# Kernel tuning notes

Measured on AMD Instinct MI355X. Metric: run time of the kernel, lower is better.

The kernel has to match this reference:

```python
import jax, jax.numpy as jnp
import numpy as np

B, S, D = 2, 2048, 1024
H = 16
HD = D // H  # 64
SCALE = HD ** -0.5


def setup_inputs() -> dict:
    key = jax.random.key(0)
    ks = jax.random.split(key, 9)
    init = lambda k, shape: jax.random.normal(k, shape, dtype=jnp.float32) * (1.0 / np.sqrt(shape[-1]))
    return {
        "x": jax.random.normal(ks[0], (B, S, D), dtype=jnp.float32),
        "wq": init(ks[1], (D, D)), "bq": jnp.zeros((D,), jnp.float32),
        "wk": init(ks[2], (D, D)), "bk": jnp.zeros((D,), jnp.float32),
        "wv": init(ks[3], (D, D)), "bv": jnp.zeros((D,), jnp.float32),
        "wo": init(ks[4], (D, D)), "bo": jnp.zeros((D,), jnp.float32),
    }


def reference(x, wq, bq, wk, bk, wv, bv, wo, bo):
    b, s, d = x.shape
    # projections -> [b, h, s, hd]
    q = (x @ wq + bq).reshape(b, s, H, HD).transpose(0, 2, 1, 3)
    k = (x @ wk + bk).reshape(b, s, H, HD).transpose(0, 2, 1, 3)
    v = (x @ wv + bv).reshape(b, s, H, HD).transpose(0, 2, 1, 3)
    # full causal attention (chunked loop in original computes exactly this)
    scores = jnp.einsum("bhqd,bhkd->bhqk", q, k) * SCALE
    causal = jnp.tril(jnp.ones((s, s), dtype=bool))
    scores = jnp.where(causal, scores, -jnp.inf)
    weights = jax.nn.softmax(scores, axis=-1)
    out = jnp.einsum("bhqk,bhkd->bhqd", weights, v)
    out = out.transpose(0, 2, 1, 3).reshape(b, s, d)
    return out @ wo + bo
```

## Files before the change

kernel.cpp:

```cpp
#include <hip/hip_runtime.h>
#include <hip/hip_bf16.h>
#include <cstdint>

#define B_  2
#define S_  2048
#define D_  1024
#define H_  16
#define HD_ 64
#define M_  (B_ * S_)
static constexpr float SC_LOG2E = 0.125f * 1.44269504088896f;

typedef __bf16 bf16x8 __attribute__((ext_vector_type(8)));
typedef float  f32x4  __attribute__((ext_vector_type(4)));

__device__ __forceinline__ unsigned short f2b(float f) {
  union { float f; unsigned u; } x; x.f = f;
  unsigned r = x.u + 0x7FFF + ((x.u >> 16) & 1);
  return (unsigned short)(r >> 16);
}

__device__ __forceinline__ void gl_lds16(const unsigned short* g, unsigned short* l) {
  __builtin_amdgcn_global_load_lds((const __attribute__((address_space(1))) void*)g,
                                   (__attribute__((address_space(3))) void*)l, 16, 0, 0);
}

__global__ void cvt_all_kernel(const float* __restrict__ x,
                               const float* __restrict__ w0, const float* __restrict__ w1,
                               const float* __restrict__ w2, const float* __restrict__ w3,
                               unsigned short* __restrict__ xb,
                               unsigned short* __restrict__ o0, unsigned short* __restrict__ o1,
                               unsigned short* __restrict__ o2, unsigned short* __restrict__ o3) {
  int tx = threadIdx.x, ty = threadIdx.y;
  if (blockIdx.z == 4) {
    int tid = ty * 32 + tx;
    int base = ((int)blockIdx.y * 32 + (int)blockIdx.x) * 1024 + tid;
    const float4* xf = (const float4*)x;
    ushort4* ob = (ushort4*)xb;
#pragma unroll
    for (int j = 0; j < 4; j++) {
      float4 v = xf[base + j * 256];
      ushort4 r;
      r.x = f2b(v.x); r.y = f2b(v.y); r.z = f2b(v.z); r.w = f2b(v.w);
      ob[base + j * 256] = r;
    }
    return;
  }
  const float* w = blockIdx.z == 0 ? w0 : blockIdx.z == 1 ? w1 : blockIdx.z == 2 ? w2 : w3;
  unsigned short* o = blockIdx.z == 0 ? o0 : blockIdx.z == 1 ? o1 : blockIdx.z == 2 ? o2 : o3;
  __shared__ float t[32][33];
  int x0 = blockIdx.x * 32, y0 = blockIdx.y * 32;
#pragma unroll
  for (int j = 0; j < 4; j++)
    t[ty + j * 8][tx] = w[(size_t)(y0 + ty + j * 8) * D_ + x0 + tx];
  __syncthreads();
#pragma unroll
  for (int j = 0; j < 4; j++)
    o[(size_t)(x0 + ty + j * 8) * D_ + y0 + tx] = f2b(t[tx][ty + j * 8]);
}

__global__ __launch_bounds__(256) void qkv_gemm_kernel(
    const unsigned short* __restrict__ xb,
    const unsigned short* __restrict__ wqt, const unsigned short* __restrict__ wkt,
    const unsigned short* __restrict__ wvt,
    const float* __restrict__ bq, const float* __restrict__ bk, const float* __restrict__ bv,
    unsigned short* __restrict__ qo, unsigned short* __restrict__ ko, unsigned short* __restrict__ vo) {
  const unsigned short* wt = blockIdx.z == 0 ? wqt : blockIdx.z == 1 ? wkt : wvt;
  const float* bias        = blockIdx.z == 0 ? bq  : blockIdx.z == 1 ? bk  : bv;
  unsigned short* out      = blockIdx.z == 0 ? qo  : blockIdx.z == 1 ? ko  : vo;
  const float scl = blockIdx.z == 0 ? SC_LOG2E : 1.0f;

  __shared__ __align__(16) unsigned short As[128 * 32];
  __shared__ __align__(16) unsigned short Bs[128 * 32];
  const int tid = threadIdx.x;
  const int lane = tid & 63, wid = tid >> 6;
  const int wm = wid & 1, wn = wid >> 1;
  const int m0 = blockIdx.x * 128, n0 = blockIdx.y * 128;
  const int l15 = lane & 15, q4 = lane >> 4;

  f32x4 zero = {0.f, 0.f, 0.f, 0.f};
  f32x4 acc[4][4];
#pragma unroll
  for (int mt = 0; mt < 4; mt++)
#pragma unroll
    for (int nt = 0; nt < 4; nt++) acc[mt][nt] = zero;

  for (int kk = 0; kk < D_; kk += 32) {
#pragma unroll
    for (int i = 0; i < 2; i++) {
      int ci = tid + i * 256;
      int row = ci >> 2, kc = ci & 3;
      gl_lds16(xb + (size_t)(m0 + row) * D_ + kk + kc * 8, As + ci * 8);
      gl_lds16(wt + (size_t)(n0 + row) * D_ + kk + kc * 8, Bs + ci * 8);
    }
    __syncthreads();
    bf16x8 af[4], bfv[4];
#pragma unroll
    for (int mt = 0; mt < 4; mt++) af[mt] = *(const bf16x8*)(As + (wm * 64 + mt * 16 + l15) * 32 + q4 * 8);
#pragma unroll
    for (int nt = 0; nt < 4; nt++) bfv[nt] = *(const bf16x8*)(Bs + (wn * 64 + nt * 16 + l15) * 32 + q4 * 8);
#pragma unroll
    for (int mt = 0; mt < 4; mt++)
#pragma unroll
      for (int nt = 0; nt < 4; nt++)
        acc[mt][nt] = __builtin_amdgcn_mfma_f32_16x16x32_bf16(af[mt], bfv[nt], acc[mt][nt], 0, 0, 0);
    __syncthreads();
  }

  if (blockIdx.z < 2) {
#pragma unroll
    for (int nt = 0; nt < 4; nt++) {
      int n = n0 + wn * 64 + nt * 16 + l15;
      float bn = bias[n];
      int h = n >> 6, hd = n & 63;
#pragma unroll
      for (int mt = 0; mt < 4; mt++) {
#pragma unroll
        for (int r = 0; r < 4; r++) {
          int m = m0 + wm * 64 + mt * 16 + q4 * 4 + r;
          int b = m >> 11, s = m & (S_ - 1);
          out[(((size_t)(b * H_ + h)) * S_ + s) * HD_ + hd] = f2b((acc[mt][nt][r] + bn) * scl);
        }
      }
    }
  } else {
    unsigned short* buf = As;
#pragma unroll
    for (int p = 0; p < 2; p++) {
      __syncthreads();
      if (wn == p) {
#pragma unroll
        for (int nt = 0; nt < 4; nt++) {
          int np = nt * 16 + l15;
          float bn = bias[n0 + p * 64 + np];
#pragma unroll
          for (int mt = 0; mt < 4; mt++)
#pragma unroll
            for (int r = 0; r < 4; r++) {
              int ml = wm * 64 + mt * 16 + q4 * 4 + r;
              buf[np * 128 + ml] = f2b(acc[mt][nt][r] + bn);
            }
        }
      }
      __syncthreads();
#pragma unroll
      for (int i = 0; i < 4; i++) {
        int ci = tid + i * 256;
        int np = ci >> 4, c = ci & 15;
        int n = n0 + p * 64 + np;
        int h = n >> 6, hd = n & 63;
        int m = m0 + c * 8;
        int b = m >> 11, s = m & (S_ - 1);
        *(uint4*)(out + (((size_t)(b * H_ + h)) * HD_ + hd) * S_ + s) = *(const uint4*)(buf + np * 128 + c * 8);
      }
    }
  }
}

__global__ __launch_bounds__(512) void attn_kernel(
    const unsigned short* __restrict__ Q, const unsigned short* __restrict__ K,
    const unsigned short* __restrict__ Vt_g, unsigned short* __restrict__ O) {
  const int bh = blockIdx.y, b = bh >> 4, h = bh & 15;
  const unsigned short* Qh = Q    + (size_t)bh * S_ * HD_;
  const unsigned short* Kh = K    + (size_t)bh * S_ * HD_;
  const unsigned short* Vh = Vt_g + (size_t)bh * HD_ * S_;

  __shared__ __align__(16) unsigned short Qs[128 * 72];
  __shared__ __align__(16) unsigned short Ks[128 * 72];
  __shared__ __align__(16) unsigned short Vt[64 * 136];
  __shared__ __align__(16) unsigned short Ps[8][16 * 136];

  const int tid = threadIdx.x, lane = tid & 63, w = tid >> 6;
  const int l15 = lane & 15, q4 = lane >> 4;
  f32x4 zero = {0.f, 0.f, 0.f, 0.f};

  const int krow0 = tid >> 3, kcol0 = (tid & 7) * 8;
  const int vrow0 = tid >> 4, vcol0 = (tid & 15) * 8;

  for (int half = 0; half < 2; half++) {
    const int qi = half ? (15 - (int)blockIdx.x) : (int)blockIdx.x;
    const int q0 = qi * 128;
    __syncthreads();
#pragma unroll
    for (int i = 0; i < 2; i++) {
      int ci = tid + i * 512, row = ci >> 3, kc = ci & 7;
      *(uint4*)(Qs + row * 72 + kc * 8) = *(const uint4*)(Qh + (size_t)(q0 + row) * HD_ + kc * 8);
    }

    float m_i = -1e30f, l_i = 0.f;
    f32x4 o_acc[4];
#pragma unroll
    for (int t = 0; t < 4; t++) o_acc[t] = zero;
    const int qrow = q0 + w * 16 + l15;
    const int nkt = qi + 1;

    uint4 kp0 = *(const uint4*)(Kh + (size_t)krow0 * HD_ + kcol0);
    uint4 kp1 = *(const uint4*)(Kh + (size_t)(krow0 + 64) * HD_ + kcol0);
    uint4 vp0 = *(const uint4*)(Vh + (size_t)vrow0 * S_ + vcol0);
    uint4 vp1 = *(const uint4*)(Vh + (size_t)(vrow0 + 32) * S_ + vcol0);

    for (int kt = 0; kt < nkt; kt++) {
      const int k0 = kt * 128;
      __syncthreads();
      *(uint4*)(Ks + krow0 * 72 + kcol0) = kp0;
      *(uint4*)(Ks + (krow0 + 64) * 72 + kcol0) = kp1;
      *(uint4*)(Vt + vrow0 * 136 + vcol0) = vp0;
      *(uint4*)(Vt + (vrow0 + 32) * 136 + vcol0) = vp1;
      if (kt + 1 < nkt) {
        int kn = k0 + 128;
        kp0 = *(const uint4*)(Kh + (size_t)(kn + krow0) * HD_ + kcol0);
        kp1 = *(const uint4*)(Kh + (size_t)(kn + krow0 + 64) * HD_ + kcol0);
        vp0 = *(const uint4*)(Vh + (size_t)vrow0 * S_ + kn + vcol0);
        vp1 = *(const uint4*)(Vh + (size_t)(vrow0 + 32) * S_ + kn + vcol0);
      }
      __syncthreads();

      bf16x8 bq0 = *(const bf16x8*)(Qs + (w * 16 + l15) * 72 + q4 * 8);
      bf16x8 bq1 = *(const bf16x8*)(Qs + (w * 16 + l15) * 72 + 32 + q4 * 8);
      f32x4 sc[8];
#pragma unroll
      for (int nt = 0; nt < 8; nt++) sc[nt] = zero;
#pragma unroll
      for (int nt = 0; nt < 8; nt++) {
        bf16x8 ak0 = *(const bf16x8*)(Ks + (nt * 16 + l15) * 72 + q4 * 8);
        bf16x8 ak1 = *(const bf16x8*)(Ks + (nt * 16 + l15) * 72 + 32 + q4 * 8);
        sc[nt] = __builtin_amdgcn_mfma_f32_16x16x32_bf16(ak0, bq0, sc[nt], 0, 0, 0);
        sc[nt] = __builtin_amdgcn_mfma_f32_16x16x32_bf16(ak1, bq1, sc[nt], 0, 0, 0);
      }

      const bool needMask = (k0 + 127) > (q0 + w * 16);
      float mx = m_i;
      if (needMask) {
#pragma unroll
        for (int nt = 0; nt < 8; nt++)
#pragma unroll
          for (int r = 0; r < 4; r++) {
            int key = k0 + nt * 16 + q4 * 4 + r;
            float v = (key > qrow) ? -1e30f : sc[nt][r];
            sc[nt][r] = v;
            mx = fmaxf(mx, v);
          }
      } else {
#pragma unroll
        for (int nt = 0; nt < 8; nt++)
#pragma unroll
          for (int r = 0; r < 4; r++) mx = fmaxf(mx, sc[nt][r]);
      }
      mx = fmaxf(mx, __shfl_xor(mx, 16));
      mx = fmaxf(mx, __shfl_xor(mx, 32));
      float alpha = __builtin_amdgcn_exp2f(m_i - mx);
      m_i = mx;
      float rs = 0.f;
#pragma unroll
      for (int nt = 0; nt < 8; nt++)
#pragma unroll
        for (int r = 0; r < 4; r++) {
          float p = __builtin_amdgcn_exp2f(sc[nt][r] - mx);
          sc[nt][r] = p;
          rs += p;
        }
      rs += __shfl_xor(rs, 16);
      rs += __shfl_xor(rs, 32);
      l_i = l_i * alpha + rs;

#pragma unroll
      for (int r = 0; r < 4; r++) {
        float ar = __shfl(alpha, q4 * 4 + r);
        o_acc[0][r] *= ar; o_acc[1][r] *= ar; o_acc[2][r] *= ar; o_acc[3][r] *= ar;
      }

#pragma unroll
      for (int nt = 0; nt < 8; nt++) {
        ushort4 pk;
        pk.x = f2b(sc[nt][0]); pk.y = f2b(sc[nt][1]);
        pk.z = f2b(sc[nt][2]); pk.w = f2b(sc[nt][3]);
        *(ushort4*)(&Ps[w][l15 * 136 + nt * 16 + q4 * 4]) = pk;
      }
      __threadfence_block();

#pragma unroll
      for (int ks = 0; ks < 4; ks++) {
        bf16x8 ap = *(const bf16x8*)(&Ps[w][l15 * 136 + ks * 32 + q4 * 8]);
#pragma unroll
        for (int nt2 = 0; nt2 < 4; nt2++) {
          bf16x8 bv = *(const bf16x8*)(Vt + (nt2 * 16 + l15) * 136 + ks * 32 + q4 * 8);
          o_acc[nt2] = __builtin_amdgcn_mfma_f32_16x16x32_bf16(ap, bv, o_acc[nt2], 0, 0, 0);
        }
      }
    }

#pragma unroll
    for (int r = 0; r < 4; r++) {
      float lr = __shfl(l_i, q4 * 4 + r);
      float inv = 1.0f / lr;
      int s = q0 + w * 16 + q4 * 4 + r;
#pragma unroll
      for (int nt2 = 0; nt2 < 4; nt2++)
        O[((size_t)(b * S_ + s)) * D_ + h * HD_ + nt2 * 16 + l15] = f2b(o_acc[nt2][r] * inv);
    }
  }
}

__global__ __launch_bounds__(256) void out_gemm_kernel(
    const unsigned short* __restrict__ ab, const unsigned short* __restrict__ wot,
    const float* __restrict__ bo, float* __restrict__ out) {
  __shared__ __align__(16) unsigned short As[128 * 32];
  __shared__ __align__(16) unsigned short Bs[128 * 32];
  const int tid = threadIdx.x;
  const int lane = tid & 63, wid = tid >> 6;
  const int wm = wid & 1, wn = wid >> 1;
  const int m0 = blockIdx.x * 128, n0 = blockIdx.y * 128;
  const int l15 = lane & 15, q4 = lane >> 4;

  f32x4 zero = {0.f, 0.f, 0.f, 0.f};
  f32x4 acc[4][4];
#pragma unroll
  for (int mt = 0; mt < 4; mt++)
#pragma unroll
    for (int nt = 0; nt < 4; nt++) acc[mt][nt] = zero;

  for (int kk = 0; kk < D_; kk += 32) {
#pragma unroll
    for (int i = 0; i < 2; i++) {
      int ci = tid + i * 256;
      int row = ci >> 2, kc = ci & 3;
      gl_lds16(ab  + (size_t)(m0 + row) * D_ + kk + kc * 8, As + ci * 8);
      gl_lds16(wot + (size_t)(n0 + row) * D_ + kk + kc * 8, Bs + ci * 8);
    }
    __syncthreads();
    bf16x8 af[4], bfv[4];
#pragma unroll
    for (int mt = 0; mt < 4; mt++) af[mt] = *(const bf16x8*)(As + (wm * 64 + mt * 16 + l15) * 32 + q4 * 8);
#pragma unroll
    for (int nt = 0; nt < 4; nt++) bfv[nt] = *(const bf16x8*)(Bs + (wn * 64 + nt * 16 + l15) * 32 + q4 * 8);
#pragma unroll
    for (int mt = 0; mt < 4; mt++)
#pragma unroll
      for (int nt = 0; nt < 4; nt++)
        acc[mt][nt] = __builtin_amdgcn_mfma_f32_16x16x32_bf16(af[mt], bfv[nt], acc[mt][nt], 0, 0, 0);
    __syncthreads();
  }

#pragma unroll
  for (int nt = 0; nt < 4; nt++) {
    int n = n0 + wn * 64 + nt * 16 + l15;
    float bn = bo[n];
#pragma unroll
    for (int mt = 0; mt < 4; mt++) {
#pragma unroll
      for (int r = 0; r < 4; r++) {
        int m = m0 + wm * 64 + mt * 16 + q4 * 4 + r;
        out[(size_t)m * D_ + n] = acc[mt][nt][r] + bn;
      }
    }
  }
}

extern "C" void kernel_launch(void* const* d_in, const int* in_sizes, int n_in,
                              void* d_out, int out_size, void* d_ws, size_t ws_size,
                              hipStream_t stream) {
  const float* x  = (const float*)d_in[0];
  const float* wq = (const float*)d_in[1];
  const float* bq = (const float*)d_in[2];
  const float* wk = (const float*)d_in[3];
  const float* bk = (const float*)d_in[4];
  const float* wv = (const float*)d_in[5];
  const float* bv = (const float*)d_in[6];
  const float* wo = (const float*)d_in[7];
  const float* bo = (const float*)d_in[8];
  float* out = (float*)d_out;

  char* ws = (char*)d_ws;
  unsigned short* xb  = (unsigned short*)(ws);
  unsigned short* wqt = (unsigned short*)(ws + (8u  << 20));
  unsigned short* wkt = (unsigned short*)(ws + (10u << 20));
  unsigned short* wvt = (unsigned short*)(ws + (12u << 20));
  unsigned short* wot = (unsigned short*)(ws + (14u << 20));
  unsigned short* qb  = (unsigned short*)(ws + (16u << 20));
  unsigned short* kb  = (unsigned short*)(ws + (24u << 20));
  unsigned short* vtg = (unsigned short*)(ws + (32u << 20));
  unsigned short* ab  = xb;

  cvt_all_kernel<<<dim3(32, 32, 5), dim3(32, 8), 0, stream>>>(x, wq, wk, wv, wo, xb, wqt, wkt, wvt, wot);
  qkv_gemm_kernel<<<dim3(32, 8, 3), dim3(256), 0, stream>>>(xb, wqt, wkt, wvt, bq, bk, bv, qb, kb, vtg);
  attn_kernel<<<dim3(8, B_ * H_), dim3(512), 0, stream>>>(qb, kb, vtg, ab);
  out_gemm_kernel<<<dim3(32, 8), dim3(256), 0, stream>>>(ab, wot, bo, out);
}
```

Before: 205.9 us.

## Double GEMM k-step per barrier; read Q/K from global directly in attention

Both projection GEMMs now load a 64-wide k-slab (two 32-wide panels per operand) per barrier pair, halving the number of sync rounds. The V transpose staging buffer gets a padded 136 stride to avoid LDS bank conflicts. The attention kernel drops the shared-memory Q and K tiles: Q fragments are held in registers once per query tile, and K fragments are loaded straight from global memory inside the MFMA loop. This removes the K prefetch and its LDS traffic, but exposes global-load latency on the critical path.

Measured after the change: 268.4 us. 30.3% more time.

```diff
diff --git a/kernel.cpp b/kernel.cpp
--- a/kernel.cpp
+++ b/kernel.cpp
@@ -69,8 +69,8 @@
   unsigned short* out      = blockIdx.z == 0 ? qo  : blockIdx.z == 1 ? ko  : vo;
   const float scl = blockIdx.z == 0 ? SC_LOG2E : 1.0f;
 
-  __shared__ __align__(16) unsigned short As[128 * 32];
-  __shared__ __align__(16) unsigned short Bs[128 * 32];
+  __shared__ __align__(16) unsigned short smem[4 * 128 * 32];
+  unsigned short* pan[4] = { smem, smem + 4096, smem + 8192, smem + 12288 };
   const int tid = threadIdx.x;
   const int lane = tid & 63, wid = tid >> 6;
   const int wm = wid & 1, wn = wid >> 1;
@@ -84,25 +84,30 @@
 #pragma unroll
     for (int nt = 0; nt < 4; nt++) acc[mt][nt] = zero;
 
-  for (int kk = 0; kk < D_; kk += 32) {
+  for (int kk = 0; kk < D_; kk += 64) {
 #pragma unroll
     for (int i = 0; i < 2; i++) {
       int ci = tid + i * 256;
       int row = ci >> 2, kc = ci & 3;
-      gl_lds16(xb + (size_t)(m0 + row) * D_ + kk + kc * 8, As + ci * 8);
-      gl_lds16(wt + (size_t)(n0 + row) * D_ + kk + kc * 8, Bs + ci * 8);
+      gl_lds16(xb + (size_t)(m0 + row) * D_ + kk      + kc * 8, pan[0] + ci * 8);
+      gl_lds16(xb + (size_t)(m0 + row) * D_ + kk + 32 + kc * 8, pan[1] + ci * 8);
+      gl_lds16(wt + (size_t)(n0 + row) * D_ + kk      + kc * 8, pan[2] + ci * 8);
+      gl_lds16(wt + (size_t)(n0 + row) * D_ + kk + 32 + kc * 8, pan[3] + ci * 8);
     }
     __syncthreads();
-    bf16x8 af[4], bfv[4];
-#pragma unroll
-    for (int mt = 0; mt < 4; mt++) af[mt] = *(const bf16x8*)(As + (wm * 64 + mt * 16 + l15) * 32 + q4 * 8);
-#pragma unroll
-    for (int nt = 0; nt < 4; nt++) bfv[nt] = *(const bf16x8*)(Bs + (wn * 64 + nt * 16 + l15) * 32 + q4 * 8);
-#pragma unroll
-    for (int mt = 0; mt < 4; mt++)
-#pragma unroll
-      for (int nt = 0; nt < 4; nt++)
-        acc[mt][nt] = __builtin_amdgcn_mfma_f32_16x16x32_bf16(af[mt], bfv[nt], acc[mt][nt], 0, 0, 0);
+#pragma unroll
+    for (int kh = 0; kh < 2; kh++) {
+      bf16x8 af[4], bfv[4];
+#pragma unroll
+      for (int mt = 0; mt < 4; mt++) af[mt]  = *(const bf16x8*)(pan[kh]     + (wm * 64 + mt * 16 + l15) * 32 + q4 * 8);
+#pragma unroll
+      for (int nt = 0; nt < 4; nt++) bfv[nt] = *(const bf16x8*)(pan[2 + kh] + (wn * 64 + nt * 16 + l15) * 32 + q4 * 8);
+#pragma unroll
+      for (int mt = 0; mt < 4; mt++)
+#pragma unroll
+        for (int nt = 0; nt < 4; nt++)
+          acc[mt][nt] = __builtin_amdgcn_mfma_f32_16x16x32_bf16(af[mt], bfv[nt], acc[mt][nt], 0, 0, 0);
+    }
     __syncthreads();
   }
 
@@ -123,7 +128,7 @@
       }
     }
   } else {
-    unsigned short* buf = As;
+    unsigned short* buf = smem;
 #pragma unroll
     for (int p = 0; p < 2; p++) {
       __syncthreads();
@@ -137,7 +142,7 @@
 #pragma unroll
             for (int r = 0; r < 4; r++) {
               int ml = wm * 64 + mt * 16 + q4 * 4 + r;
-              buf[np * 128 + ml] = f2b(acc[mt][nt][r] + bn);
+              buf[np * 136 + ml] = f2b(acc[mt][nt][r] + bn);
             }
         }
       }
@@ -150,7 +155,7 @@
         int h = n >> 6, hd = n & 63;
         int m = m0 + c * 8;
         int b = m >> 11, s = m & (S_ - 1);
-        *(uint4*)(out + (((size_t)(b * H_ + h)) * HD_ + hd) * S_ + s) = *(const uint4*)(buf + np * 128 + c * 8);
+        *(uint4*)(out + (((size_t)(b * H_ + h)) * HD_ + hd) * S_ + s) = *(const uint4*)(buf + np * 136 + c * 8);
       }
     }
   }
@@ -164,8 +169,6 @@
   const unsigned short* Kh = K    + (size_t)bh * S_ * HD_;
   const unsigned short* Vh = Vt_g + (size_t)bh * HD_ * S_;
 
-  __shared__ __align__(16) unsigned short Qs[128 * 72];
-  __shared__ __align__(16) unsigned short Ks[128 * 72];
   __shared__ __align__(16) unsigned short Vt[64 * 136];
   __shared__ __align__(16) unsigned short Ps[8][16 * 136];
 
@@ -173,18 +176,15 @@
   const int l15 = lane & 15, q4 = lane >> 4;
   f32x4 zero = {0.f, 0.f, 0.f, 0.f};
 
-  const int krow0 = tid >> 3, kcol0 = (tid & 7) * 8;
   const int vrow0 = tid >> 4, vcol0 = (tid & 15) * 8;
 
   for (int half = 0; half < 2; half++) {
     const int qi = half ? (15 - (int)blockIdx.x) : (int)blockIdx.x;
     const int q0 = qi * 128;
-    __syncthreads();
-#pragma unroll
-    for (int i = 0; i < 2; i++) {
-      int ci = tid + i * 512, row = ci >> 3, kc = ci & 7;
-      *(uint4*)(Qs + row * 72 + kc * 8) = *(const uint4*)(Qh + (size_t)(q0 + row) * HD_ + kc * 8);
-    }
+
+    const unsigned short* qp = Qh + (size_t)(q0 + w * 16 + l15) * HD_ + q4 * 8;
+    bf16x8 bq0 = *(const bf16x8*)(qp);
+    bf16x8 bq1 = *(const bf16x8*)(qp + 32);
 
     float m_i = -1e30f, l_i = 0.f;
     f32x4 o_acc[4];
@@ -193,36 +193,29 @@
     const int qrow = q0 + w * 16 + l15;
     const int nkt = qi + 1;
 
-    uint4 kp0 = *(const uint4*)(Kh + (size_t)krow0 * HD_ + kcol0);
-    uint4 kp1 = *(const uint4*)(Kh + (size_t)(krow0 + 64) * HD_ + kcol0);
     uint4 vp0 = *(const uint4*)(Vh + (size_t)vrow0 * S_ + vcol0);
     uint4 vp1 = *(const uint4*)(Vh + (size_t)(vrow0 + 32) * S_ + vcol0);
 
     for (int kt = 0; kt < nkt; kt++) {
       const int k0 = kt * 128;
       __syncthreads();
-      *(uint4*)(Ks + krow0 * 72 + kcol0) = kp0;
-      *(uint4*)(Ks + (krow0 + 64) * 72 + kcol0) = kp1;
       *(uint4*)(Vt + vrow0 * 136 + vcol0) = vp0;
       *(uint4*)(Vt + (vrow0 + 32) * 136 + vcol0) = vp1;
       if (kt + 1 < nkt) {
         int kn = k0 + 128;
-        kp0 = *(const uint4*)(Kh + (size_t)(kn + krow0) * HD_ + kcol0);
-        kp1 = *(const uint4*)(Kh + (size_t)(kn + krow0 + 64) * HD_ + kcol0);
         vp0 = *(const uint4*)(Vh + (size_t)vrow0 * S_ + kn + vcol0);
         vp1 = *(const uint4*)(Vh + (size_t)(vrow0 + 32) * S_ + kn + vcol0);
       }
       __syncthreads();
 
-      bf16x8 bq0 = *(const bf16x8*)(Qs + (w * 16 + l15) * 72 + q4 * 8);
-      bf16x8 bq1 = *(const bf16x8*)(Qs + (w * 16 + l15) * 72 + 32 + q4 * 8);
       f32x4 sc[8];
 #pragma unroll
       for (int nt = 0; nt < 8; nt++) sc[nt] = zero;
 #pragma unroll
       for (int nt = 0; nt < 8; nt++) {
-        bf16x8 ak0 = *(const bf16x8*)(Ks + (nt * 16 + l15) * 72 + q4 * 8);
-        bf16x8 ak1 = *(const bf16x8*)(Ks + (nt * 16 + l15) * 72 + 32 + q4 * 8);
+        const unsigned short* kp = Kh + (size_t)(k0 + nt * 16 + l15) * HD_ + q4 * 8;
+        bf16x8 ak0 = *(const bf16x8*)(kp);
+        bf16x8 ak1 = *(const bf16x8*)(kp + 32);
         sc[nt] = __builtin_amdgcn_mfma_f32_16x16x32_bf16(ak0, bq0, sc[nt], 0, 0, 0);
         sc[nt] = __builtin_amdgcn_mfma_f32_16x16x32_bf16(ak1, bq1, sc[nt], 0, 0, 0);
       }
@@ -303,8 +296,8 @@
 __global__ __launch_bounds__(256) void out_gemm_kernel(
     const unsigned short* __restrict__ ab, const unsigned short* __restrict__ wot,
     const float* __restrict__ bo, float* __restrict__ out) {
-  __shared__ __align__(16) unsigned short As[128 * 32];
-  __shared__ __align__(16) unsigned short Bs[128 * 32];
+  __shared__ __align__(16) unsigned short smem[4 * 128 * 32];
+  unsigned short* pan[4] = { smem, smem + 4096, smem + 8192, smem + 12288 };
   const int tid = threadIdx.x;
   const int lane = tid & 63, wid = tid >> 6;
   const int wm = wid & 1, wn = wid >> 1;
@@ -318,25 +311,30 @@
 #pragma unroll
     for (int nt = 0; nt < 4; nt++) acc[mt][nt] = zero;
 
-  for (int kk = 0; kk < D_; kk += 32) {
+  for (int kk = 0; kk < D_; kk += 64) {
 #pragma unroll
     for (int i = 0; i < 2; i++) {
       int ci = tid + i * 256;
       int row = ci >> 2, kc = ci & 3;
-      gl_lds16(ab  + (size_t)(m0 + row) * D_ + kk + kc * 8, As + ci * 8);
-      gl_lds16(wot + (size_t)(n0 + row) * D_ + kk + kc * 8, Bs + ci * 8);
+      gl_lds16(ab  + (size_t)(m0 + row) * D_ + kk      + kc * 8, pan[0] + ci * 8);
+      gl_lds16(ab  + (size_t)(m0 + row) * D_ + kk + 32 + kc * 8, pan[1] + ci * 8);
+      gl_lds16(wot + (size_t)(n0 + row) * D_ + kk      + kc * 8, pan[2] + ci * 8);
+      gl_lds16(wot + (size_t)(n0 + row) * D_ + kk + 32 + kc * 8, pan[3] + ci * 8);
     }
     __syncthreads();
-    bf16x8 af[4], bfv[4];
-#pragma unroll
-    for (int mt = 0; mt < 4; mt++) af[mt] = *(const bf16x8*)(As + (wm * 64 + mt * 16 + l15) * 32 + q4 * 8);
-#pragma unroll
-    for (int nt = 0; nt < 4; nt++) bfv[nt] = *(const bf16x8*)(Bs + (wn * 64 + nt * 16 + l15) * 32 + q4 * 8);
-#pragma unroll
-    for (int mt = 0; mt < 4; mt++)
-#pragma unroll
-      for (int nt = 0; nt < 4; nt++)
-        acc[mt][nt] = __builtin_amdgcn_mfma_f32_16x16x32_bf16(af[mt], bfv[nt], acc[mt][nt], 0, 0, 0);
+#pragma unroll
+    for (int kh = 0; kh < 2; kh++) {
+      bf16x8 af[4], bfv[4];
+#pragma unroll
+      for (int mt = 0; mt < 4; mt++) af[mt]  = *(const bf16x8*)(pan[kh]     + (wm * 64 + mt * 16 + l15) * 32 + q4 * 8);
+#pragma unroll
+      for (int nt = 0; nt < 4; nt++) bfv[nt] = *(const bf16x8*)(pan[2 + kh] + (wn * 64 + nt * 16 + l15) * 32 + q4 * 8);
+#pragma unroll
+      for (int mt = 0; mt < 4; mt++)
+#pragma unroll
+        for (int nt = 0; nt < 4; nt++)
+          acc[mt][nt] = __builtin_amdgcn_mfma_f32_16x16x32_bf16(af[mt], bfv[nt], acc[mt][nt], 0, 0, 0);
+    }
     __syncthreads();
   }
 
```
